# Kernel tuning notes

Hardware: AMD Instinct MI355X
Metric: run time of the kernel (lower is better)

The kernel has to match this reference:

```python
import jax, jax.numpy as jnp
import numpy as np

N = 50000       # nodes
E = 1600000     # directed edges (avg degree 32)
H = 2           # heads (layers 1-2)
F_IN = 128
F_HID = 64      # per-head hidden channels
F_OUT = 64
SCALE = 0.05


def setup_inputs() -> dict:
    key = jax.random.key(0)
    ks = jax.random.split(key, 15)

    def p(k, shape):
        return jax.random.normal(k, shape, jnp.float32) * SCALE

    x = jax.random.normal(ks[0], (N, F_IN), jnp.float32)
    edge_index = jax.random.randint(ks[1], (2, E), 0, N, dtype=jnp.int64)
    return dict(
        x=x,
        W1=p(ks[2], (F_IN, H * F_HID)), as1=p(ks[3], (H, F_HID)), ad1=p(ks[4], (H, F_HID)), b1=p(ks[5], (H * F_HID,)),
        W2=p(ks[6], (H * F_HID, H * F_HID)), as2=p(ks[7], (H, F_HID)), ad2=p(ks[8], (H, F_HID)), b2=p(ks[9], (H * F_HID,)),
        W3=p(ks[10], (H * F_HID, F_OUT)), as3=p(ks[11], (1, F_OUT)), ad3=p(ks[12], (1, F_OUT)), b3=p(ks[13], (F_OUT,)),
        edge_index=edge_index,
    )


def gat_layer(x, W, a_src, a_dst, b, src, dst, heads, f_out):
    """One PyG-style GATConv (concat=True, negative_slope=0.2), dropout off (eval)."""
    n = x.shape[0]
    h = (x @ W).reshape(n, heads, f_out)                 # [N,H,F]
    al_s = jnp.einsum('nhf,hf->nh', h, a_src)            # (x_j * att_src).sum(-1)
    al_d = jnp.einsum('nhf,hf->nh', h, a_dst)
    e = jax.nn.leaky_relu(al_s[src] + al_d[dst], 0.2)    # [Etot,H]
    # segment softmax over incoming edges of each dst node
    m = jax.lax.stop_gradient(jax.ops.segment_max(e, dst, num_segments=n))
    ee = jnp.exp(e - m[dst])
    denom = jax.ops.segment_sum(ee, dst, num_segments=n)
    alpha = ee / (denom[dst] + 1e-16)                    # [Etot,H]
    out = jax.ops.segment_sum(h[src] * alpha[:, :, None], dst, num_segments=n)
    return out.reshape(n, heads * f_out) + b


def reference(x, W1, as1, ad1, b1, W2, as2, ad2, b2, W3, as3, ad3, b3, edge_index):
    # add_self_loops=True (PyG default): same augmented edge set for all layers
    loops = jnp.arange(N, dtype=edge_index.dtype)
    src = jnp.concatenate([edge_index[0], loops])
    dst = jnp.concatenate([edge_index[1], loops])
    h = jax.nn.elu(gat_layer(x, W1, as1, ad1, b1, src, dst, H, F_HID))
    h = jax.nn.elu(gat_layer(h, W2, as2, ad2, b2, src, dst, H, F_HID))
    h = jax.nn.elu(gat_layer(h, W3, as3, ad3, b3, src, dst, 1, F_OUT))
    return h
```

## Files before the change

kernel.cpp:

```cpp
#include <hip/hip_runtime.h>
#include <hip/hip_bf16.h>
#include <hip/hip_fp16.h>


#define ELU(x) ((x) > 0.f ? (x) : (__expf(x) - 1.f))
#define BSH 8
#define CHK 8192

typedef _Float16 f16x8 __attribute__((ext_vector_type(8)));
typedef float    f32x4 __attribute__((ext_vector_type(4)));
typedef float    f32x2 __attribute__((ext_vector_type(2)));

__device__ inline unsigned int f16x4_to_fp8(__half2 h0, __half2 h1) {
    float2 a = __half22float2(h0), b = __half22float2(h1);
    unsigned int r = __builtin_amdgcn_cvt_pk_fp8_f32(a.x, a.y, 0, false);
    r = __builtin_amdgcn_cvt_pk_fp8_f32(b.x, b.y, r, true);
    return r;
}

__global__ __launch_bounds__(256) void phase0(
    const float* __restrict__ W1, __half* __restrict__ Wt1,
    const float* __restrict__ W2, __half* __restrict__ Wt2,
    const float* __restrict__ W3, __half* __restrict__ Wt3,
    const int* __restrict__ ei, int* __restrict__ bhist_rows, int E_)
{
    const int t = threadIdx.x;
    const int b = blockIdx.x;
    if (b < 160) {
        const float* W; __half* Wt; int N, base;
        if (b < 64)       { W = W1; Wt = Wt1; N = 128; base = b; }
        else if (b < 128) { W = W2; Wt = Wt2; N = 128; base = b - 64; }
        else              { W = W3; Wt = Wt3; N = 64;  base = b - 128; }
        int idx = base * 256 + t;
        if (idx < N * 128) {
            int nn = idx >> 7, k = idx & 127;
            Wt[idx] = __float2half(W[k * N + nn]);
        }
    } else {
        __shared__ int cnt[256];
        int hb = b - 160;
        cnt[t] = 0;
        __syncthreads();
        const int e0 = hb * CHK;
        for (int i = t; i < CHK; i += 256) {
            int e = e0 + i;
            if (e >= E_) break;
            atomicAdd(&cnt[ei[E_ + e] >> BSH], 1);
        }
        __syncthreads();
        bhist_rows[hb * 256 + t] = cnt[t];
    }
}

__global__ __launch_bounds__(256) void scan_bases(
    const int* __restrict__ bhist_rows, int* __restrict__ boff,
    int* __restrict__ bases, int* __restrict__ part, int HB, int n, int NB)
{
    __shared__ int tot[256];
    __shared__ int col[256];
    const int t = threadIdx.x;
    const int b = blockIdx.x;

    int v = 0;
    for (int r = 0; r < HB; r++) v += bhist_rows[r * 256 + t];
    int nodes_t = n - (t << BSH);
    nodes_t = nodes_t < 0 ? 0 : (nodes_t > 256 ? 256 : nodes_t);
    v = (t < NB) ? (v + nodes_t) : 0;
    tot[t] = v;
    __syncthreads();
    for (int d = 1; d < 256; d <<= 1) {
        int x = (t >= d) ? tot[t - d] : 0;
        __syncthreads();
        tot[t] += x;
        __syncthreads();
    }
    if (b == 0) {
        if (t < NB) boff[t + 1] = tot[t];
        if (t == 0) boff[0] = 0;
    }
    const int base0 = (b > 0) ? tot[b - 1] : 0;
    const int bend  = tot[b];

    int c = (t < HB) ? bhist_rows[t * 256 + b] : 0;
    col[t] = c;
    __syncthreads();
    for (int d = 1; d < 256; d <<= 1) {
        int x = (t >= d) ? col[t - d] : 0;
        __syncthreads();
        col[t] += x;
        __syncthreads();
    }
    if (t < HB) bases[b * HB + t] = base0 + col[t] - c;

    const int n0 = b << BSH;
    const int nodes = min(256, n - n0);
    const int sl0 = bend - nodes;
    if (t < nodes) part[sl0 + t] = (n0 + t) | (t << 16);
}

__global__ __launch_bounds__(256) void edge_partition(
    const int* __restrict__ ei, const int* __restrict__ bases,
    int* __restrict__ part, int E_, int HB, int NB)
{
    __shared__ int cnt[256];
    __shared__ int sbase[256];
    const int t = threadIdx.x;
    const int hb = blockIdx.x;
    cnt[t] = 0;
    sbase[t] = (t < NB) ? bases[t * HB + hb] : 0;
    __syncthreads();
    const int e0 = hb * CHK;
    for (int i = t; i < CHK; i += 256) {
        int e = e0 + i;
        if (e >= E_) break;
        int src = ei[e], dst = ei[E_ + e];
        int b = dst >> BSH;
        int pos = sbase[b] + atomicAdd(&cnt[b], 1);
        part[pos] = src | ((dst & 255) << 16);
    }
}

__global__ __launch_bounds__(256) void bucket_fill(
    const int* __restrict__ boff, const int* __restrict__ part,
    int* __restrict__ csr, int* __restrict__ off, int n)
{
    __shared__ int sm[256];
    __shared__ int cur[256];
    __shared__ int slice[12544];
    const int t = threadIdx.x;
    const int b = blockIdx.x;
    const int n0 = b << BSH;
    const int nodes = min(256, n - n0);
    const int off0 = boff[b];
    const int sz = boff[b + 1] - off0;

    cur[t] = 0;
    __syncthreads();
    for (int i = t; i < sz; i += 256)
        atomicAdd(&cur[(part[off0 + i] >> 16) & 255], 1);
    __syncthreads();
    int v = cur[t];
    sm[t] = v;
    __syncthreads();
    for (int d = 1; d < 256; d <<= 1) {
        int x = (t >= d) ? sm[t - d] : 0;
        __syncthreads();
        sm[t] += x;
        __syncthreads();
    }
    const int excl = sm[t] - v;
    if (t < nodes) off[n0 + t] = off0 + excl;
    if (t == nodes - 1) off[n0 + nodes] = off0 + sz;
    cur[t] = excl;
    __syncthreads();

    if (sz <= 12544) {
        for (int i = t; i < sz; i += 256) {
            int p  = part[off0 + i];
            int dl = (p >> 16) & 255;
            int pos = atomicAdd(&cur[dl], 1);
            slice[pos] = p & 0xFFFF;
        }
        __syncthreads();
        for (int i = t; i < sz; i += 256)
            csr[off0 + i] = slice[i];
    } else {
        for (int i = t; i < sz; i += 256) {
            int p  = part[off0 + i];
            int dl = (p >> 16) & 255;
            int pos = atomicAdd(&cur[dl], 1);
            csr[off0 + pos] = p & 0xFFFF;
        }
    }
}

__global__ __launch_bounds__(256) void gemm1_mfma(
    const float* __restrict__ A, const __half* __restrict__ Wt,
    unsigned char* __restrict__ Hout, const float* __restrict__ a_s,
    const float* __restrict__ a_d, float* __restrict__ alS,
    float* __restrict__ alD, int nrows)
{
    constexpr int N = 128, NT = 8, WR = 136;
    __shared__ _Float16 wt[N * WR];
    __shared__ _Float16 hst[4][16 * WR];

    const int t = threadIdx.x, w = t >> 6, l = t & 63;
    const int q = l >> 4, n = l & 15;
    const int node0 = blockIdx.x * 64;
    const int row_base = node0 + w * 16;

    for (int i = t; i < N * 16; i += 256) {
        int r = i >> 4, c = i & 15;
        float4 v = *(const float4*)&Wt[r * 128 + c * 8];
        *(float4*)&wt[r * WR + c * 8] = v;
    }
    __syncthreads();

    f32x4 acc[NT];
#pragma unroll
    for (int ct = 0; ct < NT; ct++) acc[ct] = (f32x4){0.f, 0.f, 0.f, 0.f};

    int arow = row_base + n; if (arow >= nrows) arow = nrows - 1;
    const float* Ap = A + (size_t)arow * 128 + q * 8;
#pragma unroll
    for (int ks = 0; ks < 4; ks++) {
        float4 va = *(const float4*)(Ap + ks * 32);
        float4 vb = *(const float4*)(Ap + ks * 32 + 4);
        f16x8 a = { (_Float16)va.x, (_Float16)va.y, (_Float16)va.z, (_Float16)va.w,
                    (_Float16)vb.x, (_Float16)vb.y, (_Float16)vb.z, (_Float16)vb.w };
#pragma unroll
        for (int ct = 0; ct < NT; ct++) {
            f16x8 bb = *(const f16x8*)&wt[(ct * 16 + n) * WR + ks * 32 + q * 8];
            acc[ct] = __builtin_amdgcn_mfma_f32_16x16x32_f16(a, bb, acc[ct], 0, 0, 0);
        }
    }

    float asv[NT], adv[NT];
#pragma unroll
    for (int ct = 0; ct < NT; ct++) {
        asv[ct] = a_s[ct * 16 + n];
        adv[ct] = a_d[ct * 16 + n];
    }
#pragma unroll
    for (int r = 0; r < 4; r++) {
        int grow = row_base + q * 4 + r;
        float s0 = 0.f, d0 = 0.f, s1 = 0.f, d1 = 0.f;
#pragma unroll
        for (int ct = 0; ct < NT; ct++) {
            float v = acc[ct][r];
            float ps = v * asv[ct], pd = v * adv[ct];
            if (ct >= 4) { s1 += ps; d1 += pd; }
            else         { s0 += ps; d0 += pd; }
        }
#pragma unroll
        for (int m = 1; m < 16; m <<= 1) {
            s0 += __shfl_xor(s0, m); d0 += __shfl_xor(d0, m);
            s1 += __shfl_xor(s1, m); d1 += __shfl_xor(d1, m);
        }
        if (n == 0 && grow < nrows) {
            alS[grow * 2] = s0;     alD[grow * 2] = d0;
            alS[grow * 2 + 1] = s1; alD[grow * 2 + 1] = d1;
        }
    }

#pragma unroll
    for (int ct = 0; ct < NT; ct++)
#pragma unroll
        for (int r = 0; r < 4; r++)
            hst[w][(q * 4 + r) * WR + ct * 16 + n] = (_Float16)acc[ct][r];
    __syncthreads();
    {
        int row = l >> 2, c = l & 3;
        int grow = row_base + row;
        if (grow < nrows) {
#pragma unroll
            for (int i = 0; i < 4; i++) {
                float4 v = *(float4*)&hst[w][row * WR + c * 32 + i * 8];
                const __half2* hp = (const __half2*)&v;
                uint2 o;
                o.x = f16x4_to_fp8(hp[0], hp[1]);
                o.y = f16x4_to_fp8(hp[2], hp[3]);
                *(uint2*)&Hout[(size_t)grow * 128 + c * 32 + i * 8] = o;
            }
        }
    }
}

template<int OUTN>
__global__ __launch_bounds__(256) void gat_gather_gemm(
    const int* __restrict__ off, const int* __restrict__ csr,
    const unsigned char* __restrict__ h, const float* __restrict__ alS,
    const float* __restrict__ alD, const float* __restrict__ bias,
    const __half* __restrict__ Wt, const float* __restrict__ a_s,
    const float* __restrict__ a_d, unsigned char* __restrict__ Hout,
    float* __restrict__ alSo, float* __restrict__ alDo, int n)
{
    constexpr int H = 2, HF = 128, WR = 136;
    constexpr int CTW = OUTN / 64;
    constexpr int CPW = OUTN / 4;
    __shared__ _Float16 actT[16 * WR];
    __shared__ float red_s[4][16], red_d[4][16];

    const int t = threadIdx.x;
    const int node0 = blockIdx.x * 16;

    const int l = t & 15;
    const int node = node0 + (t >> 4);
    const bool valid = node < n;
    const int c0 = l * 8;
    const int head = c0 >> 6;
    const int nodec = valid ? node : (n - 1);
    const float ad = alD[nodec * H + head];
    int s0 = 0, s1 = 1;
    if (valid) { s0 = off[node]; s1 = off[node + 1]; }
    const int last = s1 - 1;
    float a0 = 0.f, a1 = 0.f, a2 = 0.f, a3 = 0.f;
    float a4 = 0.f, a5 = 0.f, a6 = 0.f, a7 = 0.f, wsum = 0.f;

    float as[4];
    uint2 v[4];
    {
        int srcs[4];
#pragma unroll
        for (int k = 0; k < 4; k++) {
            int j = s0 + k;
            srcs[k] = csr[j <= last ? j : last];
        }
#pragma unroll
        for (int k = 0; k < 4; k++) {
            as[k] = alS[srcs[k] * H + head];
            v[k]  = *(const uint2*)&h[(size_t)srcs[k] * HF + c0];
        }
    }
    for (int j = s0; j < s1; j += 4) {
        int nsrc[4];
#pragma unroll
        for (int k = 0; k < 4; k++) {
            int jj = j + 4 + k;
            nsrc[k] = csr[jj <= last ? jj : last];
        }
        float nas[4];
        uint2 nv[4];
#pragma unroll
        for (int k = 0; k < 4; k++) {
            nas[k] = alS[nsrc[k] * H + head];
            nv[k]  = *(const uint2*)&h[(size_t)nsrc[k] * HF + c0];
        }
#pragma unroll
        for (int k = 0; k < 4; k++) {
            float s = as[k] + ad;
            s = s > 0.f ? s : 0.2f * s;
            float w = __expf(s);
            w = (j + k <= last) ? w : 0.f;
            f32x2 f0 = __builtin_amdgcn_cvt_pk_f32_fp8(v[k].x, false);
            f32x2 f1 = __builtin_amdgcn_cvt_pk_f32_fp8(v[k].x, true);
            f32x2 f2 = __builtin_amdgcn_cvt_pk_f32_fp8(v[k].y, false);
            f32x2 f3 = __builtin_amdgcn_cvt_pk_f32_fp8(v[k].y, true);
            a0 = fmaf(w, f0.x, a0); a1 = fmaf(w, f0.y, a1);
            a2 = fmaf(w, f1.x, a2); a3 = fmaf(w, f1.y, a3);
            a4 = fmaf(w, f2.x, a4); a5 = fmaf(w, f2.y, a5);
            a6 = fmaf(w, f3.x, a6); a7 = fmaf(w, f3.y, a7);
            wsum += w;
        }
#pragma unroll
        for (int k = 0; k < 4; k++) { as[k] = nas[k]; v[k] = nv[k]; }
    }
    {
        const float inv = 1.f / (wsum + 1e-16f);
        float4 b0 = *(const float4*)&bias[c0];
        float4 b1 = *(const float4*)&bias[c0 + 4];
        float o[8];
        o[0] = ELU(fmaf(a0, inv, b0.x));
        o[1] = ELU(fmaf(a1, inv, b0.y));
        o[2] = ELU(fmaf(a2, inv, b0.z));
        o[3] = ELU(fmaf(a3, inv, b0.w));
        o[4] = ELU(fmaf(a4, inv, b1.x));
        o[5] = ELU(fmaf(a5, inv, b1.y));
        o[6] = ELU(fmaf(a6, inv, b1.z));
        o[7] = ELU(fmaf(a7, inv, b1.w));
        __half2 p[4];
#pragma unroll
        for (int k = 0; k < 4; k++) p[k] = __floats2half2_rn(o[2 * k], o[2 * k + 1]);
        *(float4*)&actT[(t >> 4) * WR + l * 8] = *(float4*)p;
    }
    __syncthreads();

    const int w = t >> 6, l64 = t & 63, q = l64 >> 4, nn = l64 & 15;
    const __half* Wp = Wt + (w * CPW + nn) * 128 + q * 8;
    f32x4 acc[CTW];
#pragma unroll
    for (int ct = 0; ct < CTW; ct++) acc[ct] = (f32x4){0.f, 0.f, 0.f, 0.f};
#pragma unroll
    for (int ks = 0; ks < 4; ks++) {
        f16x8 a = *(const f16x8*)&actT[nn * WR + ks * 32 + q * 8];
#pragma unroll
        for (int ct = 0; ct < CTW; ct++) {
            f16x8 bb = *(const f16x8*)(Wp + ct * 16 * 128 + ks * 32);
            acc[ct] = __builtin_amdgcn_mfma_f32_16x16x32_f16(a, bb, acc[ct], 0, 0, 0);
        }
    }

    float asv[CTW], adv[CTW];
#pragma unroll
    for (int ct = 0; ct < CTW; ct++) {
        asv[ct] = a_s[w * CPW + ct * 16 + nn];
        adv[ct] = a_d[w * CPW + ct * 16 + nn];
    }
#pragma unroll
    for (int r = 0; r < 4; r++) {
        float s = 0.f, d = 0.f;
#pragma unroll
        for (int ct = 0; ct < CTW; ct++) {
            float vv = acc[ct][r];
            s = fmaf(vv, asv[ct], s);
            d = fmaf(vv, adv[ct], d);
        }
#pragma unroll
        for (int m = 1; m < 16; m <<= 1) {
            s += __shfl_xor(s, m);
            d += __shfl_xor(d, m);
        }
        if (nn == 0) { red_s[w][q * 4 + r] = s; red_d[w][q * 4 + r] = d; }
    }
    __syncthreads();

#pragma unroll
    for (int ct = 0; ct < CTW; ct++)
#pragma unroll
        for (int r = 0; r < 4; r++)
            actT[(q * 4 + r) * WR + w * CPW + ct * 16 + nn] = (_Float16)acc[ct][r];
    if (OUTN == 128) {
        if (t < 32) {
            int m = t & 15, hh = t >> 4;
            int grow = node0 + m;
            if (grow < n) {
                alSo[grow * 2 + hh] = red_s[2 * hh][m] + red_s[2 * hh + 1][m];
                alDo[grow * 2 + hh] = red_d[2 * hh][m] + red_d[2 * hh + 1][m];
            }
        }
    } else {
        if (t < 16) {
            int grow = node0 + t;
            if (grow < n) {
                alSo[grow] = red_s[0][t] + red_s[1][t] + red_s[2][t] + red_s[3][t];
                alDo[grow] = red_d[0][t] + red_d[1][t] + red_d[2][t] + red_d[3][t];
            }
        }
    }
    __syncthreads();

    if (OUTN == 128) {
        int row = t >> 4, c = t & 15;
        int grow = node0 + row;
        if (grow < n) {
            float4 v8 = *(float4*)&actT[row * WR + c * 8];
            const __half2* hp = (const __half2*)&v8;
            uint2 o;
            o.x = f16x4_to_fp8(hp[0], hp[1]);
            o.y = f16x4_to_fp8(hp[2], hp[3]);
            *(uint2*)&Hout[(size_t)grow * 128 + c * 8] = o;
        }
    } else {
        if (t < 128) {
            int row = t >> 3, c = t & 7;
            int grow = node0 + row;
            if (grow < n) {
                float4 v8 = *(float4*)&actT[row * WR + c * 8];
                const __half2* hp = (const __half2*)&v8;
                uint2 o;
                o.x = f16x4_to_fp8(hp[0], hp[1]);
                o.y = f16x4_to_fp8(hp[2], hp[3]);
                *(uint2*)&Hout[(size_t)grow * 64 + c * 8] = o;
            }
        }
    }
}

__global__ __launch_bounds__(256) void gat_gather_out(
    const int* __restrict__ off, const int* __restrict__ csr,
    const unsigned char* __restrict__ h, const float* __restrict__ alS,
    const float* __restrict__ alD, const float* __restrict__ b,
    float* __restrict__ out, int n)
{
    constexpr int HF = 64, LPN = 8, NPB = 32;
    const int l    = threadIdx.x % LPN;
    const int node = blockIdx.x * NPB + threadIdx.x / LPN;
    if (node >= n) return;
    const int c0   = l * 8;
    const float ad = alD[node];

    const int s0 = off[node], s1 = off[node + 1];
    const int last = s1 - 1;
    float a0 = 0.f, a1 = 0.f, a2 = 0.f, a3 = 0.f;
    float a4 = 0.f, a5 = 0.f, a6 = 0.f, a7 = 0.f, wsum = 0.f;

    float as[4];
    uint2 v[4];
    {
        int srcs[4];
#pragma unroll
        for (int k = 0; k < 4; k++) {
            int j = s0 + k;
            srcs[k] = csr[j <= last ? j : last];
        }
#pragma unroll
        for (int k = 0; k < 4; k++) {
            as[k] = alS[srcs[k]];
            v[k]  = *(const uint2*)&h[(size_t)srcs[k] * HF + c0];
        }
    }
    for (int j = s0; j < s1; j += 4) {
        int nsrc[4];
#pragma unroll
        for (int k = 0; k < 4; k++) {
            int jj = j + 4 + k;
            nsrc[k] = csr[jj <= last ? jj : last];
        }
        float nas[4];
        uint2 nv[4];
#pragma unroll
        for (int k = 0; k < 4; k++) {
            nas[k] = alS[nsrc[k]];
            nv[k]  = *(const uint2*)&h[(size_t)nsrc[k] * HF + c0];
        }
#pragma unroll
        for (int k = 0; k < 4; k++) {
            float s = as[k] + ad;
            s = s > 0.f ? s : 0.2f * s;
            float w = __expf(s);
            w = (j + k <= last) ? w : 0.f;
            f32x2 f0 = __builtin_amdgcn_cvt_pk_f32_fp8(v[k].x, false);
            f32x2 f1 = __builtin_amdgcn_cvt_pk_f32_fp8(v[k].x, true);
            f32x2 f2 = __builtin_amdgcn_cvt_pk_f32_fp8(v[k].y, false);
            f32x2 f3 = __builtin_amdgcn_cvt_pk_f32_fp8(v[k].y, true);
            a0 = fmaf(w, f0.x, a0); a1 = fmaf(w, f0.y, a1);
            a2 = fmaf(w, f1.x, a2); a3 = fmaf(w, f1.y, a3);
            a4 = fmaf(w, f2.x, a4); a5 = fmaf(w, f2.y, a5);
            a6 = fmaf(w, f3.x, a6); a7 = fmaf(w, f3.y, a7);
            wsum += w;
        }
#pragma unroll
        for (int k = 0; k < 4; k++) { as[k] = nas[k]; v[k] = nv[k]; }
    }

    const float inv = 1.f / (wsum + 1e-16f);
    float4 b0 = *(const float4*)&b[c0];
    float4 b1 = *(const float4*)&b[c0 + 4];
    float4 o0, o1;
    o0.x = ELU(fmaf(a0, inv, b0.x));
    o0.y = ELU(fmaf(a1, inv, b0.y));
    o0.z = ELU(fmaf(a2, inv, b0.z));
    o0.w = ELU(fmaf(a3, inv, b0.w));
    o1.x = ELU(fmaf(a4, inv, b1.x));
    o1.y = ELU(fmaf(a5, inv, b1.y));
    o1.z = ELU(fmaf(a6, inv, b1.z));
    o1.w = ELU(fmaf(a7, inv, b1.w));
    *(float4*)&out[(size_t)node * HF + c0]     = o0;
    *(float4*)&out[(size_t)node * HF + c0 + 4] = o1;
}

extern "C" void kernel_launch(void* const* d_in, const int* in_sizes, int n_in,
                              void* d_out, int out_size, void* d_ws, size_t ws_size,
                              hipStream_t stream)
{
    const float* x   = (const float*)d_in[0];
    const float* W1  = (const float*)d_in[1];
    const float* as1 = (const float*)d_in[2];
    const float* ad1 = (const float*)d_in[3];
    const float* b1  = (const float*)d_in[4];
    const float* W2  = (const float*)d_in[5];
    const float* as2 = (const float*)d_in[6];
    const float* ad2 = (const float*)d_in[7];
    const float* b2  = (const float*)d_in[8];
    const float* W3  = (const float*)d_in[9];
    const float* as3 = (const float*)d_in[10];
    const float* ad3 = (const float*)d_in[11];
    const float* b3  = (const float*)d_in[12];
    const int*   ei  = (const int*)d_in[13];
    float* out = (float*)d_out;

    const int N_   = in_sizes[0] / 128;
    const int E_   = in_sizes[13] / 2;
    const int Etot = E_ + N_;
    const int NB   = (N_ + 255) >> BSH;
    const int HB   = (E_ + CHK - 1) / CHK;

    char* ws = (char*)d_ws;
    size_t o = 0;
    auto alloc = [&](size_t bytes) { void* p = ws + o; o += (bytes + 255) & ~255ull; return p; };
    unsigned char* h1 = (unsigned char*)alloc((size_t)N_ * 128);
    unsigned char* h2 = (unsigned char*)alloc((size_t)N_ * 128);
    unsigned char* h3 = (unsigned char*)alloc((size_t)N_ * 64);
    __half* Wt1   = (__half*)alloc((size_t)128 * 128 * 2);
    __half* Wt2   = (__half*)alloc((size_t)128 * 128 * 2);
    __half* Wt3   = (__half*)alloc((size_t)64 * 128 * 2);
    float* alSa   = (float*)alloc((size_t)N_ * 2 * 4);
    float* alDa   = (float*)alloc((size_t)N_ * 2 * 4);
    float* alSb   = (float*)alloc((size_t)N_ * 2 * 4);
    float* alDb   = (float*)alloc((size_t)N_ * 2 * 4);
    int*   offb   = (int*)alloc((size_t)(N_ + 1) * 4);
    int*   bhrows = (int*)alloc((size_t)HB * 256 * 4);
    int*   boff   = (int*)alloc((size_t)257 * 4);
    int*   bases  = (int*)alloc((size_t)256 * HB * 4);
    int*   part   = (int*)alloc((size_t)Etot * 4);
    int*   csr    = (int*)alloc((size_t)Etot * 4);

    const dim3 blk(256);

    phase0<<<160 + HB, blk, 0, stream>>>(W1, Wt1, W2, Wt2, W3, Wt3, ei, bhrows, E_);
    scan_bases<<<NB, blk, 0, stream>>>(bhrows, boff, bases, part, HB, N_, NB);
    edge_partition<<<HB, blk, 0, stream>>>(ei, bases, part, E_, HB, NB);
    bucket_fill<<<NB, blk, 0, stream>>>(boff, part, csr, offb, N_);

    gemm1_mfma<<<(N_ + 63) / 64, blk, 0, stream>>>(x, Wt1, h1, as1, ad1, alSa, alDa, N_);
    gat_gather_gemm<128><<<(N_ + 15) / 16, blk, 0, stream>>>(
        offb, csr, h1, alSa, alDa, b1, Wt2, as2, ad2, h2, alSb, alDb, N_);
    gat_gather_gemm<64><<<(N_ + 15) / 16, blk, 0, stream>>>(
        offb, csr, h2, alSb, alDb, b2, Wt3, as3, ad3, h3, alSa, alDa, N_);
    gat_gather_out<<<(N_ + 31) / 32, blk, 0, stream>>>(
        offb, csr, h3, alSa, alDa, b3, out, N_);
}
```

Before: 294.1 us.

## Replace bucketed CSR build with global-atomic degree count and scatter fused with GEMM1

Replaces the four-kernel bucketed counting-sort CSR construction with a per-node degree count using global atomics, a per-bucket offset scan, and a direct atomic scatter of edges into CSR slots. The scatter blocks are merged into the same launch as the first MFMA GEMM so both run concurrently, cutting launches and removing the intermediate partition pass. In exchange the order of neighbors within each node becomes nondeterministic (fp summation order varies), and contention on global atomics for deg and off2 may be higher. A memset is added to zero the counters.

```diff
diff --git a/kernel.cpp b/kernel.cpp
--- a/kernel.cpp
+++ b/kernel.cpp
@@ -5,7 +5,6 @@
 
 #define ELU(x) ((x) > 0.f ? (x) : (__expf(x) - 1.f))
 #define BSH 8
-#define CHK 8192
 
 typedef _Float16 f16x8 __attribute__((ext_vector_type(8)));
 typedef float    f32x4 __attribute__((ext_vector_type(4)));
@@ -18,11 +17,12 @@
     return r;
 }
 
-__global__ __launch_bounds__(256) void phase0(
+__global__ __launch_bounds__(256) void prep(
     const float* __restrict__ W1, __half* __restrict__ Wt1,
     const float* __restrict__ W2, __half* __restrict__ Wt2,
     const float* __restrict__ W3, __half* __restrict__ Wt3,
-    const int* __restrict__ ei, int* __restrict__ bhist_rows, int E_)
+    const int* __restrict__ ei, int* __restrict__ deg,
+    int* __restrict__ bsum, int E_)
 {
     const int t = threadIdx.x;
     const int b = blockIdx.x;
@@ -36,158 +36,92 @@
             int nn = idx >> 7, k = idx & 127;
             Wt[idx] = __float2half(W[k * N + nn]);
         }
-    } else {
-        __shared__ int cnt[256];
-        int hb = b - 160;
-        cnt[t] = 0;
-        __syncthreads();
-        const int e0 = hb * CHK;
-        for (int i = t; i < CHK; i += 256) {
-            int e = e0 + i;
-            if (e >= E_) break;
-            atomicAdd(&cnt[ei[E_ + e] >> BSH], 1);
-        }
-        __syncthreads();
-        bhist_rows[hb * 256 + t] = cnt[t];
-    }
-}
-
-__global__ __launch_bounds__(256) void scan_bases(
-    const int* __restrict__ bhist_rows, int* __restrict__ boff,
-    int* __restrict__ bases, int* __restrict__ part, int HB, int n, int NB)
+        return;
+    }
+    __shared__ int lb[256];
+    lb[t] = 0;
+    __syncthreads();
+    const int nb = gridDim.x - 160;
+    for (int e = (b - 160) * 256 + t; e < E_; e += nb * 256) {
+        int dst = ei[E_ + e];
+        atomicAdd(&deg[dst], 1);
+        atomicAdd(&lb[dst >> BSH], 1);
+    }
+    __syncthreads();
+    if (lb[t]) atomicAdd(&bsum[t], lb[t]);
+}
+
+__global__ __launch_bounds__(256) void csr_off(
+    const int* __restrict__ deg, const int* __restrict__ bsum,
+    int* __restrict__ off, int* __restrict__ off2, int n, int NB)
 {
-    __shared__ int tot[256];
-    __shared__ int col[256];
+    __shared__ int sc[256];
     const int t = threadIdx.x;
     const int b = blockIdx.x;
 
-    int v = 0;
-    for (int r = 0; r < HB; r++) v += bhist_rows[r * 256 + t];
     int nodes_t = n - (t << BSH);
     nodes_t = nodes_t < 0 ? 0 : (nodes_t > 256 ? 256 : nodes_t);
-    v = (t < NB) ? (v + nodes_t) : 0;
-    tot[t] = v;
+    int v = (t < NB) ? (bsum[t] + nodes_t) : 0;
+    sc[t] = v;
     __syncthreads();
     for (int d = 1; d < 256; d <<= 1) {
-        int x = (t >= d) ? tot[t - d] : 0;
+        int x = (t >= d) ? sc[t - d] : 0;
         __syncthreads();
-        tot[t] += x;
+        sc[t] += x;
         __syncthreads();
     }
-    if (b == 0) {
-        if (t < NB) boff[t + 1] = tot[t];
-        if (t == 0) boff[0] = 0;
-    }
-    const int base0 = (b > 0) ? tot[b - 1] : 0;
-    const int bend  = tot[b];
-
-    int c = (t < HB) ? bhist_rows[t * 256 + b] : 0;
-    col[t] = c;
-    __syncthreads();
-    for (int d = 1; d < 256; d <<= 1) {
-        int x = (t >= d) ? col[t - d] : 0;
-        __syncthreads();
-        col[t] += x;
-        __syncthreads();
-    }
-    if (t < HB) bases[b * HB + t] = base0 + col[t] - c;
+    const int base0 = (b > 0) ? sc[b - 1] : 0;
+    __syncthreads();
 
     const int n0 = b << BSH;
     const int nodes = min(256, n - n0);
-    const int sl0 = bend - nodes;
-    if (t < nodes) part[sl0 + t] = (n0 + t) | (t << 16);
-}
-
-__global__ __launch_bounds__(256) void edge_partition(
-    const int* __restrict__ ei, const int* __restrict__ bases,
-    int* __restrict__ part, int E_, int HB, int NB)
-{
-    __shared__ int cnt[256];
-    __shared__ int sbase[256];
-    const int t = threadIdx.x;
-    const int hb = blockIdx.x;
-    cnt[t] = 0;
-    sbase[t] = (t < NB) ? bases[t * HB + hb] : 0;
-    __syncthreads();
-    const int e0 = hb * CHK;
-    for (int i = t; i < CHK; i += 256) {
-        int e = e0 + i;
-        if (e >= E_) break;
-        int src = ei[e], dst = ei[E_ + e];
-        int b = dst >> BSH;
-        int pos = sbase[b] + atomicAdd(&cnt[b], 1);
-        part[pos] = src | ((dst & 255) << 16);
-    }
-}
-
-__global__ __launch_bounds__(256) void bucket_fill(
-    const int* __restrict__ boff, const int* __restrict__ part,
-    int* __restrict__ csr, int* __restrict__ off, int n)
-{
-    __shared__ int sm[256];
-    __shared__ int cur[256];
-    __shared__ int slice[12544];
-    const int t = threadIdx.x;
-    const int b = blockIdx.x;
-    const int n0 = b << BSH;
-    const int nodes = min(256, n - n0);
-    const int off0 = boff[b];
-    const int sz = boff[b + 1] - off0;
-
-    cur[t] = 0;
-    __syncthreads();
-    for (int i = t; i < sz; i += 256)
-        atomicAdd(&cur[(part[off0 + i] >> 16) & 255], 1);
-    __syncthreads();
-    int v = cur[t];
-    sm[t] = v;
+    int d0 = (t < nodes) ? (deg[n0 + t] + 1) : 0;
+    sc[t] = d0;
     __syncthreads();
     for (int d = 1; d < 256; d <<= 1) {
-        int x = (t >= d) ? sm[t - d] : 0;
+        int x = (t >= d) ? sc[t - d] : 0;
         __syncthreads();
-        sm[t] += x;
+        sc[t] += x;
         __syncthreads();
     }
-    const int excl = sm[t] - v;
-    if (t < nodes) off[n0 + t] = off0 + excl;
-    if (t == nodes - 1) off[n0 + nodes] = off0 + sz;
-    cur[t] = excl;
-    __syncthreads();
-
-    if (sz <= 12544) {
-        for (int i = t; i < sz; i += 256) {
-            int p  = part[off0 + i];
-            int dl = (p >> 16) & 255;
-            int pos = atomicAdd(&cur[dl], 1);
-            slice[pos] = p & 0xFFFF;
-        }
-        __syncthreads();
-        for (int i = t; i < sz; i += 256)
-            csr[off0 + i] = slice[i];
-    } else {
-        for (int i = t; i < sz; i += 256) {
-            int p  = part[off0 + i];
-            int dl = (p >> 16) & 255;
-            int pos = atomicAdd(&cur[dl], 1);
-            csr[off0 + pos] = p & 0xFFFF;
-        }
-    }
-}
-
-__global__ __launch_bounds__(256) void gemm1_mfma(
+    const int excl = sc[t] - d0;
+    if (t < nodes) {
+        off[n0 + t]  = base0 + excl;
+        off2[n0 + t] = base0 + excl;
+    }
+    if (t == nodes - 1) off[n0 + nodes] = base0 + excl + d0;
+}
+
+__global__ __launch_bounds__(256) void scatter_gemm1(
+    const int* __restrict__ ei, int* __restrict__ off2, int* __restrict__ csr,
+    int E_, int n, int SB,
     const float* __restrict__ A, const __half* __restrict__ Wt,
     unsigned char* __restrict__ Hout, const float* __restrict__ a_s,
     const float* __restrict__ a_d, float* __restrict__ alS,
-    float* __restrict__ alD, int nrows)
+    float* __restrict__ alD)
 {
     constexpr int N = 128, NT = 8, WR = 136;
     __shared__ _Float16 wt[N * WR];
     __shared__ _Float16 hst[4][16 * WR];
 
-    const int t = threadIdx.x, w = t >> 6, l = t & 63;
-    const int q = l >> 4, n = l & 15;
-    const int node0 = blockIdx.x * 64;
+    const int t = threadIdx.x;
+    if ((int)blockIdx.x < SB) {
+        const int tot = E_ + n;
+        for (int i = blockIdx.x * 256 + t; i < tot; i += SB * 256) {
+            int src, dst;
+            if (i < E_) { src = ei[i]; dst = ei[E_ + i]; }
+            else        { src = i - E_; dst = src; }
+            int pos = atomicAdd(&off2[dst], 1);
+            csr[pos] = src;
+        }
+        return;
+    }
+
+    const int w = t >> 6, l = t & 63;
+    const int q = l >> 4, nn1 = l & 15;
+    const int node0 = (blockIdx.x - SB) * 64;
     const int row_base = node0 + w * 16;
+    const int nrows = n;
 
     for (int i = t; i < N * 16; i += 256) {
         int r = i >> 4, c = i & 15;
@@ -200,7 +134,7 @@
 #pragma unroll
     for (int ct = 0; ct < NT; ct++) acc[ct] = (f32x4){0.f, 0.f, 0.f, 0.f};
 
-    int arow = row_base + n; if (arow >= nrows) arow = nrows - 1;
+    int arow = row_base + nn1; if (arow >= nrows) arow = nrows - 1;
     const float* Ap = A + (size_t)arow * 128 + q * 8;
 #pragma unroll
     for (int ks = 0; ks < 4; ks++) {
@@ -210,7 +144,7 @@
                     (_Float16)vb.x, (_Float16)vb.y, (_Float16)vb.z, (_Float16)vb.w };
 #pragma unroll
         for (int ct = 0; ct < NT; ct++) {
-            f16x8 bb = *(const f16x8*)&wt[(ct * 16 + n) * WR + ks * 32 + q * 8];
+            f16x8 bb = *(const f16x8*)&wt[(ct * 16 + nn1) * WR + ks * 32 + q * 8];
             acc[ct] = __builtin_amdgcn_mfma_f32_16x16x32_f16(a, bb, acc[ct], 0, 0, 0);
         }
     }
@@ -218,8 +152,8 @@
     float asv[NT], adv[NT];
 #pragma unroll
     for (int ct = 0; ct < NT; ct++) {
-        asv[ct] = a_s[ct * 16 + n];
-        adv[ct] = a_d[ct * 16 + n];
+        asv[ct] = a_s[ct * 16 + nn1];
+        adv[ct] = a_d[ct * 16 + nn1];
     }
 #pragma unroll
     for (int r = 0; r < 4; r++) {
@@ -237,7 +171,7 @@
             s0 += __shfl_xor(s0, m); d0 += __shfl_xor(d0, m);
             s1 += __shfl_xor(s1, m); d1 += __shfl_xor(d1, m);
         }
-        if (n == 0 && grow < nrows) {
+        if (nn1 == 0 && grow < nrows) {
             alS[grow * 2] = s0;     alD[grow * 2] = d0;
             alS[grow * 2 + 1] = s1; alD[grow * 2 + 1] = d1;
         }
@@ -247,7 +181,7 @@
     for (int ct = 0; ct < NT; ct++)
 #pragma unroll
         for (int r = 0; r < 4; r++)
-            hst[w][(q * 4 + r) * WR + ct * 16 + n] = (_Float16)acc[ct][r];
+            hst[w][(q * 4 + r) * WR + ct * 16 + nn1] = (_Float16)acc[ct][r];
     __syncthreads();
     {
         int row = l >> 2, c = l & 3;
@@ -380,11 +314,11 @@
         }
     }
 
-    float asv[CTW], adv[CTW];
+    float asv[CTW], adv2[CTW];
 #pragma unroll
     for (int ct = 0; ct < CTW; ct++) {
-        asv[ct] = a_s[w * CPW + ct * 16 + nn];
-        adv[ct] = a_d[w * CPW + ct * 16 + nn];
+        asv[ct]  = a_s[w * CPW + ct * 16 + nn];
+        adv2[ct] = a_d[w * CPW + ct * 16 + nn];
     }
 #pragma unroll
     for (int r = 0; r < 4; r++) {
@@ -393,7 +327,7 @@
         for (int ct = 0; ct < CTW; ct++) {
             float vv = acc[ct][r];
             s = fmaf(vv, asv[ct], s);
-            d = fmaf(vv, adv[ct], d);
+            d = fmaf(vv, adv2[ct], d);
         }
 #pragma unroll
         for (int m = 1; m < 16; m <<= 1) {
@@ -563,7 +497,6 @@
     const int E_   = in_sizes[13] / 2;
     const int Etot = E_ + N_;
     const int NB   = (N_ + 255) >> BSH;
-    const int HB   = (E_ + CHK - 1) / CHK;
 
     char* ws = (char*)d_ws;
     size_t o = 0;
@@ -578,21 +511,25 @@
     float* alDa   = (float*)alloc((size_t)N_ * 2 * 4);
     float* alSb   = (float*)alloc((size_t)N_ * 2 * 4);
     float* alDb   = (float*)alloc((size_t)N_ * 2 * 4);
+    int*   deg    = (int*)alloc((size_t)N_ * 4);
+    int*   bsum   = (int*)alloc((size_t)256 * 4);
     int*   offb   = (int*)alloc((size_t)(N_ + 1) * 4);
-    int*   bhrows = (int*)alloc((size_t)HB * 256 * 4);
-    int*   boff   = (int*)alloc((size_t)257 * 4);
-    int*   bases  = (int*)alloc((size_t)256 * HB * 4);
-    int*   part   = (int*)alloc((size_t)Etot * 4);
+    int*   off2   = (int*)alloc((size_t)(N_ + 1) * 4);
     int*   csr    = (int*)alloc((size_t)Etot * 4);
 
     const dim3 blk(256);
-
-    phase0<<<160 + HB, blk, 0, stream>>>(W1, Wt1, W2, Wt2, W3, Wt3, ei, bhrows, E_);
-    scan_bases<<<NB, blk, 0, stream>>>(bhrows, boff, bases, part, HB, N_, NB);
-    edge_partition<<<HB, blk, 0, stream>>>(ei, bases, part, E_, HB, NB);
-    bucket_fill<<<NB, blk, 0, stream>>>(boff, part, csr, offb, N_);
-
-    gemm1_mfma<<<(N_ + 63) / 64, blk, 0, stream>>>(x, Wt1, h1, as1, ad1, alSa, alDa, N_);
+    const int G1 = (N_ + 63) / 64;
+    const int SB = 512;
+
+    size_t zlen = (size_t)((char*)(bsum + 256) - (char*)deg);
+    hipMemsetAsync(deg, 0, zlen, stream);
+
+    prep<<<160 + 784, blk, 0, stream>>>(W1, Wt1, W2, Wt2, W3, Wt3, ei, deg, bsum, E_);
+    csr_off<<<NB, blk, 0, stream>>>(deg, bsum, offb, off2, N_, NB);
+    scatter_gemm1<<<SB + G1, blk, 0, stream>>>(
+        ei, off2, csr, E_, N_, SB,
+        x, Wt1, h1, as1, ad1, alSa, alDa);
+
     gat_gather_gemm<128><<<(N_ + 15) / 16, blk, 0, stream>>>(
         offb, csr, h1, alSa, alDa, b1, Wt2, as2, ad2, h2, alSb, alDb, N_);
     gat_gather_gemm<64><<<(N_ + 15) / 16, blk, 0, stream>>>(
```

Result: slower. 414.7 us (+41.0%).

## Split fused gather+GEMM into per-head sliced gather and separate GEMM kernels

Applied to the files above, without the earlier changes.

Stores the fp8 feature tables as per-head planes of 64 bytes per node, so each gather block touches only one head's 3.2 MB plane, which is more likely to stay cache-resident. The fused gather+GEMM kernel is split into a per-head gather kernel that writes fp16 activations to a workspace buffer and a separate MFMA GEMM kernel that reads them back. CSR indices shrink to 16-bit to halve index traffic, and the activation buffer reuses the partition buffer's memory. The cost is an extra activation round-trip through global memory and two more kernel launches.

```diff
diff --git a/kernel.cpp b/kernel.cpp
--- a/kernel.cpp
+++ b/kernel.cpp
@@ -122,7 +122,7 @@
 
 __global__ __launch_bounds__(256) void bucket_fill(
     const int* __restrict__ boff, const int* __restrict__ part,
-    int* __restrict__ csr, int* __restrict__ off, int n)
+    unsigned short* __restrict__ csr, int* __restrict__ off, int n)
 {
     __shared__ int sm[256];
     __shared__ int cur[256];
@@ -163,22 +163,22 @@
         }
         __syncthreads();
         for (int i = t; i < sz; i += 256)
-            csr[off0 + i] = slice[i];
+            csr[off0 + i] = (unsigned short)slice[i];
     } else {
         for (int i = t; i < sz; i += 256) {
             int p  = part[off0 + i];
             int dl = (p >> 16) & 255;
             int pos = atomicAdd(&cur[dl], 1);
-            csr[off0 + pos] = p & 0xFFFF;
+            csr[off0 + pos] = (unsigned short)(p & 0xFFFF);
         }
     }
 }
 
 __global__ __launch_bounds__(256) void gemm1_mfma(
     const float* __restrict__ A, const __half* __restrict__ Wt,
-    unsigned char* __restrict__ Hout, const float* __restrict__ a_s,
-    const float* __restrict__ a_d, float* __restrict__ alS,
-    float* __restrict__ alD, int nrows)
+    unsigned char* __restrict__ Hout, int psz,
+    const float* __restrict__ a_s, const float* __restrict__ a_d,
+    float* __restrict__ alS, float* __restrict__ alD, int nrows)
 {
     constexpr int N = 128, NT = 8, WR = 136;
     __shared__ _Float16 wt[N * WR];
@@ -260,40 +260,33 @@
                 uint2 o;
                 o.x = f16x4_to_fp8(hp[0], hp[1]);
                 o.y = f16x4_to_fp8(hp[2], hp[3]);
-                *(uint2*)&Hout[(size_t)grow * 128 + c * 32 + i * 8] = o;
+                int cb = c * 32 + i * 8;
+                *(uint2*)&Hout[(size_t)(cb >> 6) * psz + (size_t)grow * 64 + (cb & 63)] = o;
             }
         }
     }
 }
 
-template<int OUTN>
-__global__ __launch_bounds__(256) void gat_gather_gemm(
-    const int* __restrict__ off, const int* __restrict__ csr,
-    const unsigned char* __restrict__ h, const float* __restrict__ alS,
-    const float* __restrict__ alD, const float* __restrict__ bias,
-    const __half* __restrict__ Wt, const float* __restrict__ a_s,
-    const float* __restrict__ a_d, unsigned char* __restrict__ Hout,
-    float* __restrict__ alSo, float* __restrict__ alDo, int n)
-{
-    constexpr int H = 2, HF = 128, WR = 136;
-    constexpr int CTW = OUTN / 64;
-    constexpr int CPW = OUTN / 4;
-    __shared__ _Float16 actT[16 * WR];
-    __shared__ float red_s[4][16], red_d[4][16];
-
+__global__ __launch_bounds__(256) void gslice2(
+    const int* __restrict__ off, const unsigned short* __restrict__ csr,
+    const unsigned char* __restrict__ h, int psz,
+    const float* __restrict__ alS, const float* __restrict__ alD,
+    const float* __restrict__ bias, unsigned char* __restrict__ ap,
+    int apsz, int n)
+{
+    const int g = blockIdx.x & 1;
     const int t = threadIdx.x;
-    const int node0 = blockIdx.x * 16;
-
-    const int l = t & 15;
-    const int node = node0 + (t >> 4);
+    const int l = t & 7;
+    const int node = (blockIdx.x >> 1) * 32 + (t >> 3);
     const bool valid = node < n;
     const int c0 = l * 8;
-    const int head = c0 >> 6;
     const int nodec = valid ? node : (n - 1);
-    const float ad = alD[nodec * H + head];
+    const float ad = alD[nodec * 2 + g];
     int s0 = 0, s1 = 1;
     if (valid) { s0 = off[node]; s1 = off[node + 1]; }
     const int last = s1 - 1;
+    const unsigned char* hp = h + (size_t)g * psz;
+
     float a0 = 0.f, a1 = 0.f, a2 = 0.f, a3 = 0.f;
     float a4 = 0.f, a5 = 0.f, a6 = 0.f, a7 = 0.f, wsum = 0.f;
 
@@ -308,8 +301,8 @@
         }
 #pragma unroll
         for (int k = 0; k < 4; k++) {
-            as[k] = alS[srcs[k] * H + head];
-            v[k]  = *(const uint2*)&h[(size_t)srcs[k] * HF + c0];
+            as[k] = alS[srcs[k] * 2 + g];
+            v[k]  = *(const uint2*)&hp[(size_t)srcs[k] * 64 + c0];
         }
     }
     for (int j = s0; j < s1; j += 4) {
@@ -323,8 +316,8 @@
         uint2 nv[4];
 #pragma unroll
         for (int k = 0; k < 4; k++) {
-            nas[k] = alS[nsrc[k] * H + head];
-            nv[k]  = *(const uint2*)&h[(size_t)nsrc[k] * HF + c0];
+            nas[k] = alS[nsrc[k] * 2 + g];
+            nv[k]  = *(const uint2*)&hp[(size_t)nsrc[k] * 64 + c0];
         }
 #pragma unroll
         for (int k = 0; k < 4; k++) {
@@ -345,10 +338,11 @@
 #pragma unroll
         for (int k = 0; k < 4; k++) { as[k] = nas[k]; v[k] = nv[k]; }
     }
-    {
+    if (valid) {
         const float inv = 1.f / (wsum + 1e-16f);
-        float4 b0 = *(const float4*)&bias[c0];
-        float4 b1 = *(const float4*)&bias[c0 + 4];
+        const int cf = g * 64 + c0;
+        float4 b0 = *(const float4*)&bias[cf];
+        float4 b1 = *(const float4*)&bias[cf + 4];
         float o[8];
         o[0] = ELU(fmaf(a0, inv, b0.x));
         o[1] = ELU(fmaf(a1, inv, b0.y));
@@ -361,12 +355,38 @@
         __half2 p[4];
 #pragma unroll
         for (int k = 0; k < 4; k++) p[k] = __floats2half2_rn(o[2 * k], o[2 * k + 1]);
-        *(float4*)&actT[(t >> 4) * WR + l * 8] = *(float4*)p;
+        *(float4*)&ap[(size_t)g * apsz + (size_t)node * 128 + l * 16] = *(float4*)p;
+    }
+}
+
+template<int OUTN>
+__global__ __launch_bounds__(256) void gemm_l(
+    const unsigned char* __restrict__ ap, int apsz,
+    const __half* __restrict__ Wt, const float* __restrict__ a_s,
+    const float* __restrict__ a_d, unsigned char* __restrict__ Hout,
+    int psz, float* __restrict__ alSo, float* __restrict__ alDo, int n)
+{
+    constexpr int WR = 136;
+    constexpr int CTW = OUTN / 64;
+    constexpr int CPW = OUTN / 4;
+    __shared__ _Float16 actT[16 * WR];
+    __shared__ float red_s[4][16], red_d[4][16];
+
+    const int t = threadIdx.x;
+    const int node0 = blockIdx.x * 16;
+
+    {
+        int row = t >> 4, c = t & 15;
+        int grow = node0 + row; if (grow >= n) grow = n - 1;
+        int cb2 = c * 16;
+        int pl = cb2 >> 7, o2 = cb2 & 127;
+        float4 v = *(const float4*)(ap + (size_t)pl * apsz + (size_t)grow * 128 + o2);
+        *(float4*)&actT[row * WR + c * 8] = v;
     }
     __syncthreads();
 
     const int w = t >> 6, l64 = t & 63, q = l64 >> 4, nn = l64 & 15;
-    const __half* Wp = Wt + (w * CPW + nn) * 128 + q * 8;
+    const __half* Wp = Wt + (size_t)(w * CPW + nn) * 128 + q * 8;
     f32x4 acc[CTW];
 #pragma unroll
     for (int ct = 0; ct < CTW; ct++) acc[ct] = (f32x4){0.f, 0.f, 0.f, 0.f};
@@ -380,11 +400,11 @@
         }
     }
 
-    float asv[CTW], adv[CTW];
+    float asv[CTW], adv2[CTW];
 #pragma unroll
     for (int ct = 0; ct < CTW; ct++) {
-        asv[ct] = a_s[w * CPW + ct * 16 + nn];
-        adv[ct] = a_d[w * CPW + ct * 16 + nn];
+        asv[ct]  = a_s[w * CPW + ct * 16 + nn];
+        adv2[ct] = a_d[w * CPW + ct * 16 + nn];
     }
 #pragma unroll
     for (int r = 0; r < 4; r++) {
@@ -393,7 +413,7 @@
         for (int ct = 0; ct < CTW; ct++) {
             float vv = acc[ct][r];
             s = fmaf(vv, asv[ct], s);
-            d = fmaf(vv, adv[ct], d);
+            d = fmaf(vv, adv2[ct], d);
         }
 #pragma unroll
         for (int m = 1; m < 16; m <<= 1) {
@@ -438,7 +458,8 @@
             uint2 o;
             o.x = f16x4_to_fp8(hp[0], hp[1]);
             o.y = f16x4_to_fp8(hp[2], hp[3]);
-            *(uint2*)&Hout[(size_t)grow * 128 + c * 8] = o;
+            int cb = c * 8;
+            *(uint2*)&Hout[(size_t)(cb >> 6) * psz + (size_t)grow * 64 + (cb & 63)] = o;
         }
     } else {
         if (t < 128) {
@@ -457,7 +478,7 @@
 }
 
 __global__ __launch_bounds__(256) void gat_gather_out(
-    const int* __restrict__ off, const int* __restrict__ csr,
+    const int* __restrict__ off, const unsigned short* __restrict__ csr,
     const unsigned char* __restrict__ h, const float* __restrict__ alS,
     const float* __restrict__ alD, const float* __restrict__ b,
     float* __restrict__ out, int n)
@@ -564,13 +585,16 @@
     const int Etot = E_ + N_;
     const int NB   = (N_ + 255) >> BSH;
     const int HB   = (E_ + CHK - 1) / CHK;
+    const int np   = (N_ + 255) & ~255;
+    const int psz  = np * 64;
+    const int apsz = np * 128;
 
     char* ws = (char*)d_ws;
     size_t o = 0;
     auto alloc = [&](size_t bytes) { void* p = ws + o; o += (bytes + 255) & ~255ull; return p; };
-    unsigned char* h1 = (unsigned char*)alloc((size_t)N_ * 128);
-    unsigned char* h2 = (unsigned char*)alloc((size_t)N_ * 128);
-    unsigned char* h3 = (unsigned char*)alloc((size_t)N_ * 64);
+    unsigned char* h1 = (unsigned char*)alloc((size_t)2 * psz);
+    unsigned char* h2 = (unsigned char*)alloc((size_t)2 * psz);
+    unsigned char* h3 = (unsigned char*)alloc((size_t)psz);
     __half* Wt1   = (__half*)alloc((size_t)128 * 128 * 2);
     __half* Wt2   = (__half*)alloc((size_t)128 * 128 * 2);
     __half* Wt3   = (__half*)alloc((size_t)64 * 128 * 2);
@@ -582,8 +606,12 @@
     int*   bhrows = (int*)alloc((size_t)HB * 256 * 4);
     int*   boff   = (int*)alloc((size_t)257 * 4);
     int*   bases  = (int*)alloc((size_t)256 * HB * 4);
-    int*   part   = (int*)alloc((size_t)Etot * 4);
-    int*   csr    = (int*)alloc((size_t)Etot * 4);
+    unsigned short* csr = (unsigned short*)alloc((size_t)Etot * 2);
+    size_t part_sz = (size_t)Etot * 4;
+    size_t ap_sz   = (size_t)2 * apsz;
+    void* shared = alloc(part_sz > ap_sz ? part_sz : ap_sz);
+    int* part = (int*)shared;
+    unsigned char* ap = (unsigned char*)shared;
 
     const dim3 blk(256);
 
@@ -592,11 +620,16 @@
     edge_partition<<<HB, blk, 0, stream>>>(ei, bases, part, E_, HB, NB);
     bucket_fill<<<NB, blk, 0, stream>>>(boff, part, csr, offb, N_);
 
-    gemm1_mfma<<<(N_ + 63) / 64, blk, 0, stream>>>(x, Wt1, h1, as1, ad1, alSa, alDa, N_);
-    gat_gather_gemm<128><<<(N_ + 15) / 16, blk, 0, stream>>>(
-        offb, csr, h1, alSa, alDa, b1, Wt2, as2, ad2, h2, alSb, alDb, N_);
-    gat_gather_gemm<64><<<(N_ + 15) / 16, blk, 0, stream>>>(
-        offb, csr, h2, alSb, alDb, b2, Wt3, as3, ad3, h3, alSa, alDa, N_);
+    gemm1_mfma<<<(N_ + 63) / 64, blk, 0, stream>>>(
+        x, Wt1, h1, psz, as1, ad1, alSa, alDa, N_);
+    gslice2<<<((N_ + 31) / 32) * 2, blk, 0, stream>>>(
+        offb, csr, h1, psz, alSa, alDa, b1, ap, apsz, N_);
+    gemm_l<128><<<(N_ + 15) / 16, blk, 0, stream>>>(
+        ap, apsz, Wt2, as2, ad2, h2, psz, alSb, alDb, N_);
+    gslice2<<<((N_ + 31) / 32) * 2, blk, 0, stream>>>(
+        offb, csr, h2, psz, alSb, alDb, b2, ap, apsz, N_);
+    gemm_l<64><<<(N_ + 15) / 16, blk, 0, stream>>>(
+        ap, apsz, Wt3, as3, ad3, h3, psz, alSa, alDa, N_);
     gat_gather_out<<<(N_ + 31) / 32, blk, 0, stream>>>(
         offb, csr, h3, alSa, alDa, b3, out, N_);
 }
```

After: 317.1 us. 7.8% more time.
